# Performance work log

Measured on AMD Instinct MI355X. Metric: run time of the kernel, lower is better.

Reference implementation:

```python
import jax, jax.numpy as jnp
import numpy as np

B, S, H, E = 32, 4096, 512, 512
NEG = -1000000000.0


def setup_inputs() -> dict:
    key = jax.random.key(0)
    ks = jax.random.split(key, 8)
    query = jax.random.normal(ks[0], (B, H), dtype=jnp.float32)
    keys = jax.random.normal(ks[1], (B, S, E), dtype=jnp.float32)
    mask = jax.random.randint(ks[2], (B, S), 0, 2, dtype=jnp.int32)
    # learned params (torch Linear: y = x @ W.T + b); store W already transposed
    Wq = jax.random.normal(ks[3], (H, H), dtype=jnp.float32) / np.sqrt(H)
    bq = jnp.zeros((H,), dtype=jnp.float32)
    Wk = jax.random.normal(ks[4], (E, H), dtype=jnp.float32) / np.sqrt(E)
    bk = jnp.zeros((H,), dtype=jnp.float32)
    v = jax.random.normal(ks[5], (H,), dtype=jnp.float32) / np.sqrt(H)
    bv = jnp.zeros((), dtype=jnp.float32)
    return {"query": query, "keys": keys, "mask": mask,
            "Wq": Wq, "bq": bq, "Wk": Wk, "bk": bk, "v": v, "bv": bv}


def reference(query, keys, mask, Wq, bq, Wk, bk, v, bv):
    # q_proj: (B, 1, H); k_proj: (B, S, H)
    q_proj = (query @ Wq + bq)[:, None, :]
    k_proj = jnp.einsum('bse,eh->bsh', keys, Wk) + bk
    # additive score: v^T tanh(q + k) + bv -> (B, S)
    scores = jnp.einsum('bsh,h->bs', jnp.tanh(q_proj + k_proj), v) + bv
    scores = jnp.where(mask == 0, NEG, scores)
    attn = jax.nn.softmax(scores, axis=-1)          # (B, S)
    context = jnp.einsum('bs,bse->be', attn, keys)  # (B, E)
    return context, attn
```

## Files before the change

### kernel.cpp

```cpp
#include <hip/hip_runtime.h>
#include <hip/hip_bf16.h>

#define BB 32
#define SS 4096
#define HH 512
#define EE 512
#define NCH 64
#define NEGV -1000000000.0f

using float4v = __attribute__((ext_vector_type(4))) float;
using short8v = __attribute__((ext_vector_type(8))) short;

#if defined(__has_builtin)
#if __has_builtin(__builtin_amdgcn_sched_barrier)
#define SCHED_FENCE() __builtin_amdgcn_sched_barrier(0)
#endif
#endif
#ifndef SCHED_FENCE
#define SCHED_FENCE()
#endif

__device__ inline unsigned short f2bf(float x) {
    union { float f; unsigned int u; } c; c.f = x;
    unsigned int r = c.u + 0x7FFFu + ((c.u >> 16) & 1u);
    return (unsigned short)(r >> 16);
}
__device__ inline float bf2f(unsigned short s) {
    union { float f; unsigned int u; } c; c.u = ((unsigned int)s) << 16;
    return c.f;
}
__device__ inline unsigned int pk2bf(float a, float b) {
    union { __hip_bfloat162 h; unsigned int u; } c;
    c.h = __float22bfloat162_rn(float2{a, b});
    return c.u;
}

__global__ void qproj_kernel(const float* __restrict__ query, const float* __restrict__ Wq,
                             float* __restrict__ qp) {
    __shared__ float qs[64];
    int b = blockIdx.y, e0 = blockIdx.x * 64, t = threadIdx.x;
    if (t < 64) qs[t] = query[b * HH + e0 + t];
    __syncthreads();
    int h0 = t, h1 = t + 256;
    float a0 = 0.f, a1 = 0.f;
    #pragma unroll 8
    for (int e = 0; e < 64; ++e) {
        float q = qs[e];
        a0 += q * Wq[(size_t)(e0 + e) * HH + h0];
        a1 += q * Wq[(size_t)(e0 + e) * HH + h1];
    }
    atomicAdd(&qp[b * HH + h0], a0);
    atomicAdd(&qp[b * HH + h1], a1);
}

__global__ void wkt_kernel(const float* __restrict__ Wk, unsigned short* __restrict__ WkT) {
    int g = blockIdx.x * 256 + threadIdx.x;
    int lane = g & 63, nt = (g >> 6) & 31, ks = g >> 11;
    int lq = lane >> 4, lr = lane & 15;
    int h = nt * 16 + lr;
    int e0 = ks * 32 + lq * 8;
    short8v o;
    #pragma unroll
    for (int j = 0; j < 8; ++j) o[j] = (short)f2bf(Wk[(size_t)(e0 + j) * HH + h]);
    *(short8v*)(WkT + (size_t)g * 8) = o;
}

__launch_bounds__(512, 4)
__global__ void fused_kernel(const float* __restrict__ keys, const unsigned short* __restrict__ WkT,
                             const float* __restrict__ qp, const float* __restrict__ bq,
                             const float* __restrict__ bk, const float* __restrict__ v,
                             const float* __restrict__ bv, const int* __restrict__ mask,
                             float* __restrict__ scores, float* __restrict__ part,
                             float* __restrict__ marr, float* __restrict__ larr) {
    constexpr int LDK = EE + 8;
    __shared__ unsigned short klds[64 * LDK];
    __shared__ float qp_lds[HH];
    __shared__ float v_lds[HH];
    __shared__ float red[8][64];
    __shared__ float p_lds[64];
    int b = blockIdx.y, c = blockIdx.x, s0 = c * 64;
    int tid = threadIdx.x;

    for (int i = tid; i < HH; i += 512) {
        qp_lds[i] = qp[b * HH + i] + bq[i] + bk[i];
        v_lds[i] = v[i];
    }

    const float4v* ksrc = (const float4v*)(keys + ((size_t)b * SS + s0) * EE);
    int srow = tid >> 3 << 0;
    (void)srow;

    float4v kv[4];
    #pragma unroll
    for (int p = 0; p < 4; ++p) {
        int idx = tid + p * 512;
        kv[p] = ksrc[(size_t)(idx >> 5) * 128 + (idx & 31)];
    }
    #pragma unroll
    for (int p = 0; p < 4; ++p) {
        int idx = tid + p * 512, row = idx >> 5, c4 = idx & 31;
        *(unsigned int*)(&klds[row * LDK + c4 * 4])     = pk2bf(kv[p].x, kv[p].y);
        *(unsigned int*)(&klds[row * LDK + c4 * 4 + 2]) = pk2bf(kv[p].z, kv[p].w);
    }
    __syncthreads();

    int w = tid >> 6, lane = tid & 63;
    int lq = lane >> 4, lr = lane & 15;
    int nt0 = w * 4;

    float4v acc[4][4];
    #pragma unroll
    for (int m = 0; m < 4; ++m)
        #pragma unroll
        for (int j = 0; j < 4; ++j) acc[m][j] = (float4v){0.f, 0.f, 0.f, 0.f};

    const short8v* Wf = (const short8v*)WkT;

    for (int q = 0; q < 4; ++q) {
        if (q < 3) {
            #pragma unroll
            for (int p = 0; p < 4; ++p) {
                int idx = tid + p * 512;
                kv[p] = ksrc[(size_t)(idx >> 5) * 128 + (q + 1) * 32 + (idx & 31)];
            }
        }
        SCHED_FENCE();
        #pragma unroll
        for (int ksl = 0; ksl < 4; ++ksl) {
            int kq = q * 4 + ksl;
            short8v bfrag[4];
            #pragma unroll
            for (int j = 0; j < 4; ++j)
                bfrag[j] = Wf[((size_t)kq * 32 + nt0 + j) * 64 + lane];
            #pragma unroll
            for (int m = 0; m < 4; ++m) {
                short8v afrag = *(const short8v*)(&klds[(m * 16 + lr) * LDK + kq * 32 + lq * 8]);
                #pragma unroll
                for (int j = 0; j < 4; ++j)
                    acc[m][j] = __builtin_amdgcn_mfma_f32_16x16x32_bf16(afrag, bfrag[j], acc[m][j], 0, 0, 0);
            }
        }
        if (q < 3) {
            #pragma unroll
            for (int p = 0; p < 4; ++p) {
                int idx = tid + p * 512, row = idx >> 5, c4 = (q + 1) * 32 + (idx & 31);
                *(unsigned int*)(&klds[row * LDK + c4 * 4])     = pk2bf(kv[p].x, kv[p].y);
                *(unsigned int*)(&klds[row * LDK + c4 * 4 + 2]) = pk2bf(kv[p].z, kv[p].w);
            }
            __syncthreads();
        }
    }

    float part_r[4][4];
    #pragma unroll
    for (int m = 0; m < 4; ++m)
        #pragma unroll
        for (int r = 0; r < 4; ++r) part_r[m][r] = 0.f;
    #pragma unroll
    for (int j = 0; j < 4; ++j) {
        int h = (nt0 + j) * 16 + lr;
        float vj = v_lds[h], qj = qp_lds[h], vj2 = -2.f * vj;
        #pragma unroll
        for (int m = 0; m < 4; ++m) {
            #pragma unroll
            for (int r = 0; r < 4; ++r) {
                float x = qj + acc[m][j][r];
                float rr = __frcp_rn(__expf(2.f * x) + 1.f);
                part_r[m][r] += __builtin_fmaf(vj2, rr, vj);
            }
        }
    }
    #pragma unroll
    for (int m = 0; m < 4; ++m)
        #pragma unroll
        for (int r = 0; r < 4; ++r) {
            float p = part_r[m][r];
            p += __shfl_xor(p, 1, 16);
            p += __shfl_xor(p, 2, 16);
            p += __shfl_xor(p, 4, 16);
            p += __shfl_xor(p, 8, 16);
            part_r[m][r] = p;
        }
    if (lr == 0) {
        #pragma unroll
        for (int m = 0; m < 4; ++m)
            #pragma unroll
            for (int r = 0; r < 4; ++r)
                red[w][m * 16 + lq * 4 + r] = part_r[m][r];
    }
    __syncthreads();

    if (tid < 64) {
        float sc = red[0][tid] + red[1][tid] + red[2][tid] + red[3][tid]
                 + red[4][tid] + red[5][tid] + red[6][tid] + red[7][tid] + bv[0];
        int s = s0 + tid;
        if (mask[b * SS + s] == 0) sc = NEGV;
        scores[b * SS + s] = sc;
        float mv = sc;
        #pragma unroll
        for (int off = 1; off < 64; off <<= 1) mv = fmaxf(mv, __shfl_xor(mv, off));
        float pe = __expf(sc - mv);
        float ls = pe;
        #pragma unroll
        for (int off = 1; off < 64; off <<= 1) ls += __shfl_xor(ls, off);
        p_lds[tid] = pe;
        if (tid == 0) { marr[b * NCH + c] = mv; larr[b * NCH + c] = ls; }
    }
    __syncthreads();

    {
        float o0 = 0.f, o1 = 0.f;
        #pragma unroll 8
        for (int s = 0; s < 32; ++s) {
            o0 += p_lds[s]      * bf2f(klds[s * LDK + tid]);
            o1 += p_lds[s + 32] * bf2f(klds[(s + 32) * LDK + tid]);
        }
        part[((size_t)b * NCH + c) * EE + tid] = o0 + o1;
    }
}

__global__ void finalize_kernel(const float* __restrict__ scores, const float* __restrict__ part,
                                const float* __restrict__ marr, const float* __restrict__ larr,
                                float* __restrict__ ctx, float* __restrict__ attn) {
    __shared__ float wgt[NCH];
    __shared__ float Ms, Ls;
    int b = blockIdx.y, px = blockIdx.x, t = threadIdx.x;
    if (t < NCH) {
        float m = marr[b * NCH + t], l = larr[b * NCH + t];
        float M = m;
        #pragma unroll
        for (int off = 1; off < 64; off <<= 1) M = fmaxf(M, __shfl_xor(M, off));
        float wq = __expf(m - M);
        float L = wq * l;
        #pragma unroll
        for (int off = 1; off < 64; off <<= 1) L += __shfl_xor(L, off);
        wgt[t] = wq;
        if (t == 0) { Ms = M; Ls = L; }
    }
    __syncthreads();
    float M = Ms, invL = 1.f / Ls;
    if (px == 0) {
        float o = 0.f;
        #pragma unroll 8
        for (int cc = 0; cc < NCH; ++cc)
            o += wgt[cc] * part[((size_t)b * NCH + cc) * EE + t];
        ctx[b * EE + t] = o * invL;
    }
    int s0 = px * 1024;
    attn[b * SS + s0 + t]       = __expf(scores[b * SS + s0 + t] - M) * invL;
    attn[b * SS + s0 + t + 512] = __expf(scores[b * SS + s0 + t + 512] - M) * invL;
}

extern "C" void kernel_launch(void* const* d_in, const int* in_sizes, int n_in,
                              void* d_out, int out_size, void* d_ws, size_t ws_size,
                              hipStream_t stream) {
    const float* query = (const float*)d_in[0];
    const float* keys  = (const float*)d_in[1];
    const int*   mask  = (const int*)d_in[2];
    const float* Wq    = (const float*)d_in[3];
    const float* bq    = (const float*)d_in[4];
    const float* Wk    = (const float*)d_in[5];
    const float* bk    = (const float*)d_in[6];
    const float* v     = (const float*)d_in[7];
    const float* bv    = (const float*)d_in[8];

    float* out  = (float*)d_out;
    float* ctx  = out;
    float* attn = out + BB * EE;

    char* ws = (char*)d_ws;
    float* qp           = (float*)ws;
    unsigned short* WkT = (unsigned short*)(ws + 65536);
    float* scores       = (float*)(ws + 589824);
    float* part         = (float*)(ws + 1114112);
    float* marr         = (float*)(ws + 5308416);
    float* larr         = (float*)(ws + 5316608);

    hipMemsetAsync(qp, 0, BB * HH * sizeof(float), stream);
    qproj_kernel<<<dim3(8, BB), 256, 0, stream>>>(query, Wq, qp);
    wkt_kernel<<<128, 256, 0, stream>>>(Wk, WkT);
    fused_kernel<<<dim3(NCH, BB), 512, 0, stream>>>(keys, WkT, qp, bq, bk, v, bv, mask,
                                                    scores, part, marr, larr);
    finalize_kernel<<<dim3(4, BB), 512, 0, stream>>>(scores, part, marr, larr, ctx, attn);
}
```

Measured before the change: 425.1 us.

## Merge prep kernels, prefetch Wk fragments, store exp-scores, use fast reciprocal

Merges the query projection and Wk transpose into one prep kernel that writes four partial projections instead of using a memset and atomics, removing two launches. The fused kernel now prefetches the next B fragments one k-step ahead, raises wave priority around the MFMA block, loads the mask early, packs the LDS writes into 64-bit stores, and uses a hardware rcp in the tanh path. It stores the per-chunk exp values directly, so finalize only rescales them by the chunk weight instead of recomputing the exp. The prefetch adds register pressure under launch bounds of 4, and the approximate rcp slightly changes numerics.

```diff
diff --git a/kernel.cpp b/kernel.cpp
--- a/kernel.cpp
+++ b/kernel.cpp
@@ -15,9 +15,21 @@
 #if __has_builtin(__builtin_amdgcn_sched_barrier)
 #define SCHED_FENCE() __builtin_amdgcn_sched_barrier(0)
 #endif
+#if __has_builtin(__builtin_amdgcn_rcpf)
+#define FAST_RCP(x) __builtin_amdgcn_rcpf(x)
+#endif
+#if __has_builtin(__builtin_amdgcn_s_setprio)
+#define SETPRIO(n) __builtin_amdgcn_s_setprio(n)
+#endif
 #endif
 #ifndef SCHED_FENCE
 #define SCHED_FENCE()
+#endif
+#ifndef FAST_RCP
+#define FAST_RCP(x) (1.0f / (x))
+#endif
+#ifndef SETPRIO
+#define SETPRIO(n)
 #endif
 
 __device__ inline unsigned short f2bf(float x) {
@@ -35,42 +47,44 @@
     return c.u;
 }
 
-__global__ void qproj_kernel(const float* __restrict__ query, const float* __restrict__ Wq,
-                             float* __restrict__ qp) {
-    __shared__ float qs[64];
-    int b = blockIdx.y, e0 = blockIdx.x * 64, t = threadIdx.x;
-    if (t < 64) qs[t] = query[b * HH + e0 + t];
-    __syncthreads();
-    int h0 = t, h1 = t + 256;
-    float a0 = 0.f, a1 = 0.f;
-    #pragma unroll 8
-    for (int e = 0; e < 64; ++e) {
-        float q = qs[e];
-        a0 += q * Wq[(size_t)(e0 + e) * HH + h0];
-        a1 += q * Wq[(size_t)(e0 + e) * HH + h1];
-    }
-    atomicAdd(&qp[b * HH + h0], a0);
-    atomicAdd(&qp[b * HH + h1], a1);
-}
-
-__global__ void wkt_kernel(const float* __restrict__ Wk, unsigned short* __restrict__ WkT) {
-    int g = blockIdx.x * 256 + threadIdx.x;
-    int lane = g & 63, nt = (g >> 6) & 31, ks = g >> 11;
-    int lq = lane >> 4, lr = lane & 15;
-    int h = nt * 16 + lr;
-    int e0 = ks * 32 + lq * 8;
-    short8v o;
-    #pragma unroll
-    for (int j = 0; j < 8; ++j) o[j] = (short)f2bf(Wk[(size_t)(e0 + j) * HH + h]);
-    *(short8v*)(WkT + (size_t)g * 8) = o;
+__global__ void prep_kernel(const float* __restrict__ query, const float* __restrict__ Wq,
+                            float* __restrict__ qp4,
+                            const float* __restrict__ Wk, unsigned short* __restrict__ WkT) {
+    int bx = blockIdx.x, t = threadIdx.x;
+    if (bx < 4 * BB) {
+        __shared__ float qs[128];
+        int b = bx >> 2, seg = bx & 3;
+        if (t < 128) qs[t] = query[b * HH + seg * 128 + t];
+        __syncthreads();
+        float a0 = 0.f, a1 = 0.f;
+        const float* wq = Wq + (size_t)(seg * 128) * HH;
+        #pragma unroll 8
+        for (int e = 0; e < 128; ++e) {
+            float q = qs[e];
+            a0 += q * wq[(size_t)e * HH + t];
+            a1 += q * wq[(size_t)e * HH + t + 256];
+        }
+        qp4[((size_t)seg * BB + b) * HH + t] = a0;
+        qp4[((size_t)seg * BB + b) * HH + t + 256] = a1;
+    } else {
+        int g = (bx - 4 * BB) * 256 + t;
+        int lane = g & 63, nt = (g >> 6) & 31, ks = g >> 11;
+        int lq = lane >> 4, lr = lane & 15;
+        int h = nt * 16 + lr;
+        int e0 = ks * 32 + lq * 8;
+        short8v o;
+        #pragma unroll
+        for (int j = 0; j < 8; ++j) o[j] = (short)f2bf(Wk[(size_t)(e0 + j) * HH + h]);
+        *(short8v*)(WkT + (size_t)g * 8) = o;
+    }
 }
 
 __launch_bounds__(512, 4)
 __global__ void fused_kernel(const float* __restrict__ keys, const unsigned short* __restrict__ WkT,
-                             const float* __restrict__ qp, const float* __restrict__ bq,
+                             const float* __restrict__ qp4, const float* __restrict__ bq,
                              const float* __restrict__ bk, const float* __restrict__ v,
                              const float* __restrict__ bv, const int* __restrict__ mask,
-                             float* __restrict__ scores, float* __restrict__ part,
+                             float* __restrict__ pe_out, float* __restrict__ part,
                              float* __restrict__ marr, float* __restrict__ larr) {
     constexpr int LDK = EE + 8;
     __shared__ unsigned short klds[64 * LDK];
@@ -81,32 +95,38 @@
     int b = blockIdx.y, c = blockIdx.x, s0 = c * 64;
     int tid = threadIdx.x;
 
-    for (int i = tid; i < HH; i += 512) {
-        qp_lds[i] = qp[b * HH + i] + bq[i] + bk[i];
-        v_lds[i] = v[i];
-    }
-
     const float4v* ksrc = (const float4v*)(keys + ((size_t)b * SS + s0) * EE);
-    int srow = tid >> 3 << 0;
-    (void)srow;
-
     float4v kv[4];
     #pragma unroll
     for (int p = 0; p < 4; ++p) {
         int idx = tid + p * 512;
         kv[p] = ksrc[(size_t)(idx >> 5) * 128 + (idx & 31)];
     }
+    int mval = 0;
+    if (tid < 64) mval = mask[b * SS + s0 + tid];
+
+    for (int i = tid; i < HH; i += 512) {
+        qp_lds[i] = qp4[((size_t)0 * BB + b) * HH + i] + qp4[((size_t)1 * BB + b) * HH + i]
+                  + qp4[((size_t)2 * BB + b) * HH + i] + qp4[((size_t)3 * BB + b) * HH + i]
+                  + bq[i] + bk[i];
+        v_lds[i] = v[i];
+    }
+
     #pragma unroll
     for (int p = 0; p < 4; ++p) {
         int idx = tid + p * 512, row = idx >> 5, c4 = idx & 31;
-        *(unsigned int*)(&klds[row * LDK + c4 * 4])     = pk2bf(kv[p].x, kv[p].y);
-        *(unsigned int*)(&klds[row * LDK + c4 * 4 + 2]) = pk2bf(kv[p].z, kv[p].w);
-    }
-    __syncthreads();
+        unsigned int u0 = pk2bf(kv[p].x, kv[p].y), u1 = pk2bf(kv[p].z, kv[p].w);
+        *(uint2*)(&klds[row * LDK + c4 * 4]) = make_uint2(u0, u1);
+    }
 
     int w = tid >> 6, lane = tid & 63;
     int lq = lane >> 4, lr = lane & 15;
     int nt0 = w * 4;
+    const short8v* Wf = (const short8v*)WkT;
+
+    short8v bcur[4];
+    #pragma unroll
+    for (int j = 0; j < 4; ++j) bcur[j] = Wf[(size_t)(nt0 + j) * 64 + lane];
 
     float4v acc[4][4];
     #pragma unroll
@@ -114,8 +134,9 @@
         #pragma unroll
         for (int j = 0; j < 4; ++j) acc[m][j] = (float4v){0.f, 0.f, 0.f, 0.f};
 
-    const short8v* Wf = (const short8v*)WkT;
-
+    __syncthreads();
+
+    #pragma unroll
     for (int q = 0; q < 4; ++q) {
         if (q < 3) {
             #pragma unroll
@@ -128,24 +149,32 @@
         #pragma unroll
         for (int ksl = 0; ksl < 4; ++ksl) {
             int kq = q * 4 + ksl;
-            short8v bfrag[4];
-            #pragma unroll
-            for (int j = 0; j < 4; ++j)
-                bfrag[j] = Wf[((size_t)kq * 32 + nt0 + j) * 64 + lane];
+            short8v bn[4];
+            if (kq < 15) {
+                #pragma unroll
+                for (int j = 0; j < 4; ++j)
+                    bn[j] = Wf[((size_t)(kq + 1) * 32 + nt0 + j) * 64 + lane];
+            }
+            SETPRIO(1);
             #pragma unroll
             for (int m = 0; m < 4; ++m) {
                 short8v afrag = *(const short8v*)(&klds[(m * 16 + lr) * LDK + kq * 32 + lq * 8]);
                 #pragma unroll
                 for (int j = 0; j < 4; ++j)
-                    acc[m][j] = __builtin_amdgcn_mfma_f32_16x16x32_bf16(afrag, bfrag[j], acc[m][j], 0, 0, 0);
+                    acc[m][j] = __builtin_amdgcn_mfma_f32_16x16x32_bf16(afrag, bcur[j], acc[m][j], 0, 0, 0);
+            }
+            SETPRIO(0);
+            if (kq < 15) {
+                #pragma unroll
+                for (int j = 0; j < 4; ++j) bcur[j] = bn[j];
             }
         }
         if (q < 3) {
             #pragma unroll
             for (int p = 0; p < 4; ++p) {
                 int idx = tid + p * 512, row = idx >> 5, c4 = (q + 1) * 32 + (idx & 31);
-                *(unsigned int*)(&klds[row * LDK + c4 * 4])     = pk2bf(kv[p].x, kv[p].y);
-                *(unsigned int*)(&klds[row * LDK + c4 * 4 + 2]) = pk2bf(kv[p].z, kv[p].w);
+                unsigned int u0 = pk2bf(kv[p].x, kv[p].y), u1 = pk2bf(kv[p].z, kv[p].w);
+                *(uint2*)(&klds[row * LDK + c4 * 4]) = make_uint2(u0, u1);
             }
             __syncthreads();
         }
@@ -165,7 +194,7 @@
             #pragma unroll
             for (int r = 0; r < 4; ++r) {
                 float x = qj + acc[m][j][r];
-                float rr = __frcp_rn(__expf(2.f * x) + 1.f);
+                float rr = FAST_RCP(__expf(x + x) + 1.f);
                 part_r[m][r] += __builtin_fmaf(vj2, rr, vj);
             }
         }
@@ -193,9 +222,7 @@
     if (tid < 64) {
         float sc = red[0][tid] + red[1][tid] + red[2][tid] + red[3][tid]
                  + red[4][tid] + red[5][tid] + red[6][tid] + red[7][tid] + bv[0];
-        int s = s0 + tid;
-        if (mask[b * SS + s] == 0) sc = NEGV;
-        scores[b * SS + s] = sc;
+        if (mval == 0) sc = NEGV;
         float mv = sc;
         #pragma unroll
         for (int off = 1; off < 64; off <<= 1) mv = fmaxf(mv, __shfl_xor(mv, off));
@@ -204,6 +231,7 @@
         #pragma unroll
         for (int off = 1; off < 64; off <<= 1) ls += __shfl_xor(ls, off);
         p_lds[tid] = pe;
+        pe_out[b * SS + s0 + tid] = pe;
         if (tid == 0) { marr[b * NCH + c] = mv; larr[b * NCH + c] = ls; }
     }
     __syncthreads();
@@ -219,11 +247,11 @@
     }
 }
 
-__global__ void finalize_kernel(const float* __restrict__ scores, const float* __restrict__ part,
+__global__ void finalize_kernel(const float* __restrict__ pe_arr, const float* __restrict__ part,
                                 const float* __restrict__ marr, const float* __restrict__ larr,
                                 float* __restrict__ ctx, float* __restrict__ attn) {
     __shared__ float wgt[NCH];
-    __shared__ float Ms, Ls;
+    __shared__ float Ls;
     int b = blockIdx.y, px = blockIdx.x, t = threadIdx.x;
     if (t < NCH) {
         float m = marr[b * NCH + t], l = larr[b * NCH + t];
@@ -235,10 +263,10 @@
         #pragma unroll
         for (int off = 1; off < 64; off <<= 1) L += __shfl_xor(L, off);
         wgt[t] = wq;
-        if (t == 0) { Ms = M; Ls = L; }
+        if (t == 0) Ls = L;
     }
     __syncthreads();
-    float M = Ms, invL = 1.f / Ls;
+    float invL = 1.f / Ls;
     if (px == 0) {
         float o = 0.f;
         #pragma unroll 8
@@ -247,8 +275,8 @@
         ctx[b * EE + t] = o * invL;
     }
     int s0 = px * 1024;
-    attn[b * SS + s0 + t]       = __expf(scores[b * SS + s0 + t] - M) * invL;
-    attn[b * SS + s0 + t + 512] = __expf(scores[b * SS + s0 + t + 512] - M) * invL;
+    attn[b * SS + s0 + t]       = pe_arr[b * SS + s0 + t]       * wgt[(s0 + t) >> 6]       * invL;
+    attn[b * SS + s0 + t + 512] = pe_arr[b * SS + s0 + t + 512] * wgt[(s0 + t + 512) >> 6] * invL;
 }
 
 extern "C" void kernel_launch(void* const* d_in, const int* in_sizes, int n_in,
@@ -269,17 +297,15 @@
     float* attn = out + BB * EE;
 
     char* ws = (char*)d_ws;
-    float* qp           = (float*)ws;
-    unsigned short* WkT = (unsigned short*)(ws + 65536);
-    float* scores       = (float*)(ws + 589824);
-    float* part         = (float*)(ws + 1114112);
-    float* marr         = (float*)(ws + 5308416);
-    float* larr         = (float*)(ws + 5316608);
-
-    hipMemsetAsync(qp, 0, BB * HH * sizeof(float), stream);
-    qproj_kernel<<<dim3(8, BB), 256, 0, stream>>>(query, Wq, qp);
-    wkt_kernel<<<128, 256, 0, stream>>>(Wk, WkT);
-    fused_kernel<<<dim3(NCH, BB), 512, 0, stream>>>(keys, WkT, qp, bq, bk, v, bv, mask,
-                                                    scores, part, marr, larr);
-    finalize_kernel<<<dim3(4, BB), 512, 0, stream>>>(scores, part, marr, larr, ctx, attn);
-}
+    float* qp4          = (float*)ws;
+    unsigned short* WkT = (unsigned short*)(ws + 262144);
+    float* pe           = (float*)(ws + 786432);
+    float* part         = (float*)(ws + 1310720);
+    float* marr         = (float*)(ws + 5505024);
+    float* larr         = (float*)(ws + 5513216);
+
+    prep_kernel<<<256, 256, 0, stream>>>(query, Wq, qp4, Wk, WkT);
+    fused_kernel<<<dim3(NCH, BB), 512, 0, stream>>>(keys, WkT, qp4, bq, bk, v, bv, mask,
+                                                    pe, part, marr, larr);
+    finalize_kernel<<<dim3(4, BB), 512, 0, stream>>>(pe, part, marr, larr, ctx, attn);
+}
```

Result: faster. 414.3 us (-2.5%).
